# Performance work log

Hardware: AMD Instinct MI355X
Metric: run time of the kernel (lower is better)

The kernel has to match this reference:

```python
import jax, jax.numpy as jnp
import numpy as np

NUM_HEADS = 16

def rotate_half(x):
    h = x.shape[-1] // 2
    return jnp.concatenate([-x[..., h:], x[..., :h]], axis=-1)

def setup_inputs() -> dict:
    key = jax.random.key(0)
    k1, k2, k3 = jax.random.split(key, 3)
    B, S, H = 2, 2048, 1024
    x = jax.random.normal(k1, (B, S, H), dtype=jnp.float32)
    W_qkv = jax.random.normal(k2, (3 * H, H), dtype=jnp.float32) * (1.0 / np.sqrt(H))
    W_proj = jax.random.normal(k3, (H, H), dtype=jnp.float32) * (1.0 / np.sqrt(H))
    return {"x": x, "W_qkv": W_qkv, "W_proj": W_proj}

def reference(x, W_qkv, W_proj):
    B, S, H = x.shape
    nH = NUM_HEADS
    hd = H // nH
    # QKV projection (bias=False): y = x @ W.T
    qkv = jnp.einsum('bsh,oh->bso', x, W_qkv)  # [B,S,3H]
    q, k, v = jnp.split(qkv, 3, axis=-1)
    def to_heads(t):
        return t.reshape(B, S, nH, hd).transpose(0, 2, 1, 3)  # [B,nH,S,hd]
    q, k, v = to_heads(q), to_heads(k), to_heads(v)
    # RoPE on first half of head_dim; freqs dim = hd//2
    half = hd // 2
    inv_freq = 1.0 / (10000.0 ** (jnp.arange(0, hd, 2, dtype=jnp.float32) / hd))  # [hd//2]
    t = jnp.arange(S, dtype=jnp.float32)
    freqs = t[:, None] * inv_freq[None, :]  # [S, hd//2]
    cos = jnp.cos(freqs)[None, None]  # [1,1,S,hd//2]
    sin = jnp.sin(freqs)[None, None]
    q_half, q_rest = q[..., :half], q[..., half:]
    k_half, k_rest = k[..., :half], k[..., half:]
    q_rot = q_half * cos + rotate_half(q_half) * sin
    k_rot = k_half * cos + rotate_half(k_half) * sin
    q = jnp.concatenate([q_rot, q_rest], axis=-1)
    k = jnp.concatenate([k_rot, k_rest], axis=-1)
    # scaled dot-product attention (no mask, dropout=0 / eval)
    scale = 1.0 / np.sqrt(hd)
    att = jnp.einsum('bhqd,bhkd->bhqk', q, k) * scale  # [B,nH,S,S]
    att = jax.nn.softmax(att, axis=-1)
    out = jnp.einsum('bhqk,bhkd->bhqd', att, v)  # [B,nH,S,hd]
    out = out.transpose(0, 2, 1, 3).reshape(B, S, H)
    return jnp.einsum('bsh,oh->bso', out, W_proj)
```

## Files before the change

kernel.cpp:

```cpp
#include <hip/hip_runtime.h>
#include <math.h>

#define SEQ  2048
#define NHD  16
#define HD   64
#define HDIM 1024

typedef short s16x8 __attribute__((ext_vector_type(8)));
typedef short s16x4 __attribute__((ext_vector_type(4)));
typedef float f32x4 __attribute__((ext_vector_type(4)));

typedef const __attribute__((address_space(1))) unsigned int* gp_t;
typedef __attribute__((address_space(3))) unsigned int* lp_t;

__device__ __forceinline__ void async16(const short* g, short* l) {
    __builtin_amdgcn_global_load_lds((gp_t)g, (lp_t)l, 16, 0, 0);
}

__device__ __forceinline__ short f2bf(float f) {
    unsigned int u = __float_as_uint(f);
    u += 0x7fff + ((u >> 16) & 1);
    return (short)(u >> 16);
}
__device__ __forceinline__ float bf2f(short s) {
    return __uint_as_float(((unsigned int)(unsigned short)s) << 16);
}
__device__ __forceinline__ unsigned pkbf(float a, float b) {
    unsigned ua = __float_as_uint(a) + 0x8000u;
    unsigned ub = __float_as_uint(b) + 0x8000u;
    return __builtin_amdgcn_perm(ua, ub, 0x03020706u);
}

__global__ void detect_k(const unsigned short* __restrict__ x, int* __restrict__ flag) {
    int cnt = 0;
    #pragma unroll 4
    for (int j = 0; j < 32; ++j) {
        unsigned short h = x[threadIdx.x * 32 + j];
        int e = (h >> 7) & 0xFF;
        cnt += (e >= 100 && e <= 140) ? 1 : 0;
    }
    __shared__ int tot;
    if (threadIdx.x == 0) tot = 0;
    __syncthreads();
    atomicAdd(&tot, cnt);
    __syncthreads();
    if (threadIdx.x == 0) *flag = (tot > (8192 * 9) / 10) ? 1 : 0;
}

#define XG4  (4096 * 1024 / 4)
#define WQG4 (3072 * 1024 / 4)
#define WPG4 (1024 * 1024 / 4)
__global__ void cvt_all_k(const void* __restrict__ xr, const void* __restrict__ wqr,
                          const void* __restrict__ wpr, short* __restrict__ xo,
                          short* __restrict__ wqo, short* __restrict__ wpo,
                          const int* __restrict__ flag) {
    int i = blockIdx.x * 256 + threadIdx.x;
    const void* in; short* out; int j;
    if (i < XG4)             { in = xr;  out = xo;  j = i; }
    else if (i < XG4 + WQG4) { in = wqr; out = wqo; j = i - XG4; }
    else                     { in = wpr; out = wpo; j = i - XG4 - WQG4; }
    if (*flag) {
        ((s16x4*)out)[j] = ((const s16x4*)in)[j];
    } else {
        f32x4 v = ((const f32x4*)in)[j];
        union { unsigned u[2]; s16x4 v; } r;
        r.u[0] = pkbf(v[0], v[1]);
        r.u[1] = pkbf(v[2], v[3]);
        ((s16x4*)out)[j] = r.v;
    }
}

__global__ void rope_tab_k(float2* __restrict__ tab) {
    int i = blockIdx.x * 256 + threadIdx.x;
    if (i >= SEQ * 32) return;
    int s = i >> 5, d = i & 31;
    float invf = (float)pow(10000.0, -(double)d / 32.0);
    float af = (float)s * invf;
    double a = (double)af;
    tab[i] = make_float2((float)cos(a), (float)sin(a));
}

template<int MODE>
__global__ __launch_bounds__(256, 2)
void gemm_bt(const short* __restrict__ A, const short* __restrict__ B,
             short* __restrict__ q, short* __restrict__ kbuf, short* __restrict__ vt,
             float* __restrict__ C, const float2* __restrict__ tab,
             int K, int N) {
    __shared__ __align__(16) short As[2][128 * 32];
    __shared__ __align__(16) short Bs[2][128 * 32];
    const int tid  = threadIdx.x;
    const int w    = tid >> 6, lane = tid & 63;
    const int quad = lane >> 4, l16 = lane & 15;
    const int wm = (w >> 1) * 64, wn = (w & 1) * 64;
    const int rowA0 = blockIdx.y * 128;
    const int colB0 = blockIdx.x * 128;

    auto stage = [&](int buf, int kb) {
        #pragma unroll
        for (int i = 0; i < 2; ++i) {
            int cidx = i * 256 + w * 64 + lane;
            int row = cidx >> 2, sc = cidx & 3;
            int c = sc ^ (row & 3);
            async16(&A[(long)(rowA0 + row) * K + kb + c * 8],
                    &As[buf][(i * 256 + w * 64) * 8]);
            async16(&B[(long)(colB0 + row) * K + kb + c * 8],
                    &Bs[buf][(i * 256 + w * 64) * 8]);
        }
    };

    f32x4 acc[4][4] = {};
    stage(0, 0);

    for (int kb = 0, it = 0; kb < K; kb += 32, ++it) {
        const int cur = it & 1;
        __syncthreads();
        if (kb + 32 < K) stage(cur ^ 1, kb + 32);

        s16x8 af[4], bfr[4];
        const int slot = quad ^ (l16 & 3);
        #pragma unroll
        for (int mi = 0; mi < 4; ++mi)
            af[mi] = *(const s16x8*)&As[cur][(wm + mi * 16 + l16) * 32 + slot * 8];
        #pragma unroll
        for (int ni = 0; ni < 4; ++ni)
            bfr[ni] = *(const s16x8*)&Bs[cur][(wn + ni * 16 + l16) * 32 + slot * 8];
        #pragma unroll
        for (int mi = 0; mi < 4; ++mi)
            #pragma unroll
            for (int ni = 0; ni < 4; ++ni)
                acc[mi][ni] = __builtin_amdgcn_mfma_f32_16x16x32_bf16(
                    af[mi], bfr[ni], acc[mi][ni], 0, 0, 0);
    }

    const int cb = colB0 + wn;
    if (MODE == 1) {
        #pragma unroll
        for (int mi = 0; mi < 4; ++mi) {
            #pragma unroll
            for (int r = 0; r < 4; ++r) {
                int gm = rowA0 + wm + mi * 16 + quad * 4 + r;
                float* cp = C + (long)gm * N + cb + l16;
                #pragma unroll
                for (int ni = 0; ni < 4; ++ni)
                    cp[ni * 16] = acc[mi][ni][r];
            }
        }
        return;
    }
    const int sector = cb >> 10;
    const int head   = (cb & 1023) >> 6;
    const int gmb = rowA0 + wm;
    const int b = gmb >> 11, s0 = gmb & 2047;
    __syncthreads();
    short* arena = (w < 2) ? (&As[0][0] + w * 4096) : (&Bs[0][0] + (w - 2) * 4096);
    auto aw = [&](int row, int col, short val) {
        arena[row * 64 + (((col >> 3) ^ (row & 7)) << 3) + (col & 7)] = val;
    };
    if (sector < 2) {
        const float sc = (sector == 0) ? 0.18033688f : 1.0f;
        #pragma unroll
        for (int mi = 0; mi < 4; ++mi) {
            #pragma unroll
            for (int r = 0; r < 4; ++r) {
                int lrow = mi * 16 + quad * 4 + r;
                int s = s0 + lrow;
                float v0 = acc[mi][0][r], v1 = acc[mi][1][r];
                float v2 = acc[mi][2][r], v3 = acc[mi][3][r];
                float2 cs0 = tab[s * 32 + l16];
                float2 cs1 = tab[s * 32 + 16 + l16];
                float n0 = v0 * cs0.x - v1 * cs0.y;
                float n1 = v1 * cs1.x + v0 * cs1.y;
                aw(lrow, l16,      f2bf(n0 * sc));
                aw(lrow, l16 + 16, f2bf(n1 * sc));
                aw(lrow, l16 + 32, f2bf(v2 * sc));
                aw(lrow, l16 + 48, f2bf(v3 * sc));
            }
        }
        short* dst0 = (sector == 0 ? q : kbuf)
                    + ((long)((b * NHD + head) * SEQ + s0)) * HD;
        #pragma unroll
        for (int it = 0; it < 8; ++it) {
            int row = it * 8 + (lane >> 3), cc = lane & 7;
            s16x8 vv = *(const s16x8*)&arena[row * 64 + ((cc ^ (row & 7)) << 3)];
            *(s16x8*)&dst0[row * HD + cc * 8] = vv;
        }
    } else {
        #pragma unroll
        for (int mi = 0; mi < 4; ++mi) {
            #pragma unroll
            for (int r = 0; r < 4; ++r) {
                int scol = mi * 16 + quad * 4 + r;
                aw(l16,      scol, f2bf(acc[mi][0][r]));
                aw(l16 + 16, scol, f2bf(acc[mi][1][r]));
                aw(l16 + 32, scol, f2bf(acc[mi][2][r]));
                aw(l16 + 48, scol, f2bf(acc[mi][3][r]));
            }
        }
        short* dstv = vt + ((long)((b * NHD + head) * HD)) * SEQ + s0;
        #pragma unroll
        for (int it = 0; it < 8; ++it) {
            int dd = it * 8 + (lane >> 3), so8 = lane & 7;
            s16x8 vv = *(const s16x8*)&arena[dd * 64 + ((so8 ^ (dd & 7)) << 3)];
            *(s16x8*)&dstv[(long)dd * SEQ + so8 * 8] = vv;
        }
    }
}

__global__ __launch_bounds__(256, 4)
void flash_attn(const short* __restrict__ Q, const short* __restrict__ K,
                const short* __restrict__ Vt, short* __restrict__ opart,
                float* __restrict__ lpart, int nt) {
    __shared__ __align__(16) short Ks[2][64 * 64];
    __shared__ __align__(16) short Vs[2][64 * 64];
    const int tid  = threadIdx.x;
    const int w    = tid >> 6, lane = tid & 63;
    const int quad = lane >> 4, l16 = lane & 15;
    const int bh = blockIdx.x >> 1;
    const int z  = blockIdx.x & 1;
    const int qb = blockIdx.y * 128;
    const short* Qp = Q  + (long)bh * SEQ * HD + (long)qb * HD;
    const short* Kp = K  + (long)bh * SEQ * HD;
    const short* Vp = Vt + (long)bh * HD * SEQ;
    const int kt0 = z * nt;

    auto stage = [&](int buf, int kt) {
        #pragma unroll
        for (int i = 0; i < 2; ++i) {
            int cidx = i * 256 + w * 64 + lane;
            int row = cidx >> 3, sc = cidx & 7;
            int c = sc ^ (row & 7);
            async16(&Kp[(kt * 64 + row) * HD + c * 8],
                    &Ks[buf][(i * 256 + w * 64) * 8]);
            async16(&Vp[(long)row * SEQ + kt * 64 + c * 8],
                    &Vs[buf][(i * 256 + w * 64) * 8]);
        }
    };

    s16x8 aq[2][2];
    #pragma unroll
    for (int mi = 0; mi < 2; ++mi)
        #pragma unroll
        for (int ks = 0; ks < 2; ++ks)
            aq[mi][ks] = *(const s16x8*)&Qp[(w * 32 + mi * 16 + l16) * HD
                                            + ks * 32 + quad * 8];

    s16x8 ones8;
    #pragma unroll
    for (int j = 0; j < 8; ++j) ones8[j] = (short)0x3F80;

    f32x4 oacc[2][4] = {};
    f32x4 lacc[2] = {};

    stage(0, kt0);
    for (int it = 0; it < nt; ++it) {
        const int cur = it & 1;
        __syncthreads();
        if (it + 1 < nt) stage(cur ^ 1, kt0 + it + 1);

        f32x4 st[2][4] = {};
        #pragma unroll
        for (int ki = 0; ki < 4; ++ki) {
            s16x8 ak0 = *(const s16x8*)&Ks[cur][(ki * 16 + l16) * 64 + (quad ^ (l16 & 7)) * 8];
            s16x8 ak1 = *(const s16x8*)&Ks[cur][(ki * 16 + l16) * 64 + ((4 + quad) ^ (l16 & 7)) * 8];
            #pragma unroll
            for (int mi = 0; mi < 2; ++mi) {
                st[mi][ki] = __builtin_amdgcn_mfma_f32_16x16x32_bf16(
                    ak0, aq[mi][0], st[mi][ki], 0, 0, 0);
                st[mi][ki] = __builtin_amdgcn_mfma_f32_16x16x32_bf16(
                    ak1, aq[mi][1], st[mi][ki], 0, 0, 0);
            }
        }

        s16x8 bp[2][2];
        #pragma unroll
        for (int mi = 0; mi < 2; ++mi)
            #pragma unroll
            for (int t = 0; t < 2; ++t) {
                union { unsigned u[4]; s16x8 v; } pk;
                pk.u[0] = pkbf(exp2f(st[mi][2 * t][0]),     exp2f(st[mi][2 * t][1]));
                pk.u[1] = pkbf(exp2f(st[mi][2 * t][2]),     exp2f(st[mi][2 * t][3]));
                pk.u[2] = pkbf(exp2f(st[mi][2 * t + 1][0]), exp2f(st[mi][2 * t + 1][1]));
                pk.u[3] = pkbf(exp2f(st[mi][2 * t + 1][2]), exp2f(st[mi][2 * t + 1][3]));
                bp[mi][t] = pk.v;
            }

        #pragma unroll
        for (int t = 0; t < 2; ++t) {
            #pragma unroll
            for (int nd = 0; nd < 4; ++nd) {
                int d = nd * 16 + l16;
                s16x4 va = *(const s16x4*)&Vs[cur][d * 64
                             + ((4 * t + (quad >> 1)) ^ (l16 & 7)) * 8
                             + (quad & 1) * 4];
                s16x4 vb = *(const s16x4*)&Vs[cur][d * 64
                             + ((4 * t + 2 + (quad >> 1)) ^ (l16 & 7)) * 8
                             + (quad & 1) * 4];
                s16x8 av = {va[0], va[1], va[2], va[3],
                            vb[0], vb[1], vb[2], vb[3]};
                #pragma unroll
                for (int mi = 0; mi < 2; ++mi)
                    oacc[mi][nd] = __builtin_amdgcn_mfma_f32_16x16x32_bf16(
                        av, bp[mi][t], oacc[mi][nd], 0, 0, 0);
            }
            #pragma unroll
            for (int mi = 0; mi < 2; ++mi)
                lacc[mi] = __builtin_amdgcn_mfma_f32_16x16x32_bf16(
                    ones8, bp[mi][t], lacc[mi], 0, 0, 0);
        }
    }

    #pragma unroll
    for (int mi = 0; mi < 2; ++mi) {
        int srow = qb + w * 32 + mi * 16 + l16;
        long prow = (long)(z * 2 * NHD + bh) * SEQ + srow;
        if (quad == 0) lpart[prow] = lacc[mi][0];
        short* op = opart + prow * 64 + quad * 4;
        #pragma unroll
        for (int nd = 0; nd < 4; ++nd) {
            union { unsigned u[2]; s16x4 v; } pk;
            pk.u[0] = pkbf(oacc[mi][nd][0], oacc[mi][nd][1]);
            pk.u[1] = pkbf(oacc[mi][nd][2], oacc[mi][nd][3]);
            *(s16x4*)&op[nd * 16] = pk.v;
        }
    }
}

__global__ __launch_bounds__(256)
void merge_k(const short* __restrict__ opart, const float* __restrict__ lpart,
             short* __restrict__ att) {
    int idx = blockIdx.x * 256 + threadIdx.x;
    int t16 = idx & 15, rowg = idx >> 4;
    int bh = rowg >> 11, srow = rowg & 2047;
    float inv = 1.0f / (lpart[rowg] + lpart[65536 + rowg]);
    s16x4 o1 = *(const s16x4*)&opart[(long)rowg * 64 + t16 * 4];
    s16x4 o2 = *(const s16x4*)&opart[(long)(65536 + rowg) * 64 + t16 * 4];
    int b = bh >> 4, h = bh & 15;
    short* dst = att + ((long)(b * SEQ + srow)) * HDIM + h * HD + t16 * 4;
    union { unsigned u[2]; s16x4 v; } r;
    r.u[0] = pkbf((bf2f(o1[0]) + bf2f(o2[0])) * inv,
                  (bf2f(o1[1]) + bf2f(o2[1])) * inv);
    r.u[1] = pkbf((bf2f(o1[2]) + bf2f(o2[2])) * inv,
                  (bf2f(o1[3]) + bf2f(o2[3])) * inv);
    *(s16x4*)dst = r.v;
}

extern "C" void kernel_launch(void* const* d_in, const int* in_sizes, int n_in,
                              void* d_out, int out_size, void* d_ws, size_t ws_size,
                              hipStream_t stream) {
    const void* x_raw  = d_in[0];
    const void* Wq_raw = d_in[1];
    const void* Wp_raw = d_in[2];
    for (int i = 0; i < n_in; ++i) {
        if      (in_sizes[i] == 4096 * 1024) x_raw  = d_in[i];
        else if (in_sizes[i] == 3072 * 1024) Wq_raw = d_in[i];
        else if (in_sizes[i] == 1024 * 1024) Wp_raw = d_in[i];
    }
    float* out = (float*)d_out;

    const size_t MB = 1u << 20;
    char* ws = (char*)d_ws;
    short*  q     = (short*)(ws);
    short*  k     = (short*)(ws +  8 * MB);
    short*  vt    = (short*)(ws + 16 * MB);
    short*  xbf   = (short*)(ws + 24 * MB);
    short*  att   = xbf;
    short*  wqkv  = (short*)(ws + 32 * MB);
    short*  wprj  = (short*)(ws + 38 * MB);
    float2* tab   = (float2*)(ws + 40 * MB);
    int*    flag  = (int*)(ws + 40 * MB + 512 * 1024);
    short*  opart = (short*)(ws + 41 * MB);
    float*  lprt  = (float*)(ws + 57 * MB);

    detect_k<<<dim3(1), dim3(256), 0, stream>>>((const unsigned short*)x_raw, flag);

    cvt_all_k<<<dim3((XG4 + WQG4 + WPG4) / 256), dim3(256), 0, stream>>>(
        x_raw, Wq_raw, Wp_raw, xbf, wqkv, wprj, flag);

    rope_tab_k<<<dim3(SEQ * 32 / 256), dim3(256), 0, stream>>>(tab);

    gemm_bt<0><<<dim3(3072 / 128, 4096 / 128), dim3(256), 0, stream>>>(
        xbf, wqkv, q, k, vt, (float*)nullptr, tab, 1024, 3072);

    flash_attn<<<dim3(2 * NHD * 2, SEQ / 128), dim3(256), 0, stream>>>(
        q, k, vt, opart, lprt, 16);

    merge_k<<<dim3(65536 * 16 / 256), dim3(256), 0, stream>>>(opart, lprt, att);

    gemm_bt<1><<<dim3(1024 / 128, 4096 / 128), dim3(256), 0, stream>>>(
        att, wprj, (short*)nullptr, (short*)nullptr, (short*)nullptr, out, tab, 1024, 1024);
}
```

Before: 205.3 us.

## Fuse dtype detection, conversion and RoPE table into one kernel; trim attention inner loop

Merges the separate detect, convert and RoPE-table kernels into a single launch, with each conversion block deciding bf16-vs-fp32 input from a ballot over its own data instead of a global flag. This removes two kernel launches and their serialization. In flash attention the first MFMA of each score tile now takes a zero accumulator instead of a zero-initialised array, and exp2f is replaced by the raw hardware exp2 builtin. The per-block detection heuristic could classify blocks inconsistently, and the hardware exp2 may differ slightly in precision and denormal handling.

```diff
diff --git a/kernel.cpp b/kernel.cpp
--- a/kernel.cpp
+++ b/kernel.cpp
@@ -31,35 +31,38 @@
     return __builtin_amdgcn_perm(ua, ub, 0x03020706u);
 }
 
-__global__ void detect_k(const unsigned short* __restrict__ x, int* __restrict__ flag) {
-    int cnt = 0;
-    #pragma unroll 4
-    for (int j = 0; j < 32; ++j) {
-        unsigned short h = x[threadIdx.x * 32 + j];
-        int e = (h >> 7) & 0xFF;
-        cnt += (e >= 100 && e <= 140) ? 1 : 0;
-    }
-    __shared__ int tot;
-    if (threadIdx.x == 0) tot = 0;
-    __syncthreads();
-    atomicAdd(&tot, cnt);
-    __syncthreads();
-    if (threadIdx.x == 0) *flag = (tot > (8192 * 9) / 10) ? 1 : 0;
-}
-
 #define XG4  (4096 * 1024 / 4)
 #define WQG4 (3072 * 1024 / 4)
 #define WPG4 (1024 * 1024 / 4)
-__global__ void cvt_all_k(const void* __restrict__ xr, const void* __restrict__ wqr,
-                          const void* __restrict__ wpr, short* __restrict__ xo,
-                          short* __restrict__ wqo, short* __restrict__ wpo,
-                          const int* __restrict__ flag) {
-    int i = blockIdx.x * 256 + threadIdx.x;
+#define NCVT ((XG4 + WQG4 + WPG4) / 256)
+__global__ void cvt_rope_k(const void* __restrict__ xr, const void* __restrict__ wqr,
+                           const void* __restrict__ wpr, short* __restrict__ xo,
+                           short* __restrict__ wqo, short* __restrict__ wpo,
+                           float2* __restrict__ tab) {
+    const int tid = threadIdx.x;
+    if (blockIdx.x >= NCVT) {
+        int i = (blockIdx.x - NCVT) * 256 + tid;
+        int s = i >> 5, d = i & 31;
+        float invf = (float)pow(10000.0, -(double)d / 32.0);
+        float af = (float)s * invf;
+        tab[i] = make_float2((float)cos((double)af), (float)sin((double)af));
+        return;
+    }
+    int i = blockIdx.x * 256 + tid;
     const void* in; short* out; int j;
     if (i < XG4)             { in = xr;  out = xo;  j = i; }
     else if (i < XG4 + WQG4) { in = wqr; out = wqo; j = i - XG4; }
     else                     { in = wpr; out = wpo; j = i - XG4 - WQG4; }
-    if (*flag) {
+    const int jbase = j - tid;
+    unsigned short h = ((const unsigned short*)in)[(size_t)jbase * 4 + tid];
+    int e = (h >> 7) & 0xFF;
+    unsigned long long b = __ballot(e >= 100 && e <= 140);
+    __shared__ int tot;
+    if (tid == 0) tot = 0;
+    __syncthreads();
+    if ((tid & 63) == 0) atomicAdd(&tot, __popcll(b));
+    __syncthreads();
+    if (tot > 230) {
         ((s16x4*)out)[j] = ((const s16x4*)in)[j];
     } else {
         f32x4 v = ((const f32x4*)in)[j];
@@ -68,16 +71,6 @@
         r.u[1] = pkbf(v[2], v[3]);
         ((s16x4*)out)[j] = r.v;
     }
-}
-
-__global__ void rope_tab_k(float2* __restrict__ tab) {
-    int i = blockIdx.x * 256 + threadIdx.x;
-    if (i >= SEQ * 32) return;
-    int s = i >> 5, d = i & 31;
-    float invf = (float)pow(10000.0, -(double)d / 32.0);
-    float af = (float)s * invf;
-    double a = (double)af;
-    tab[i] = make_float2((float)cos(a), (float)sin(a));
 }
 
 template<int MODE>
@@ -248,6 +241,7 @@
     #pragma unroll
     for (int j = 0; j < 8; ++j) ones8[j] = (short)0x3F80;
 
+    const f32x4 z4 = {};
     f32x4 oacc[2][4] = {};
     f32x4 lacc[2] = {};
 
@@ -256,16 +250,18 @@
         const int cur = it & 1;
         __syncthreads();
         if (it + 1 < nt) stage(cur ^ 1, kt0 + it + 1);
-
-        f32x4 st[2][4] = {};
+        const short* kcur = Ks[cur];
+        const short* vcur = Vs[cur];
+
+        f32x4 st[2][4];
         #pragma unroll
         for (int ki = 0; ki < 4; ++ki) {
-            s16x8 ak0 = *(const s16x8*)&Ks[cur][(ki * 16 + l16) * 64 + (quad ^ (l16 & 7)) * 8];
-            s16x8 ak1 = *(const s16x8*)&Ks[cur][(ki * 16 + l16) * 64 + ((4 + quad) ^ (l16 & 7)) * 8];
+            s16x8 ak0 = *(const s16x8*)&kcur[(ki * 16 + l16) * 64 + (quad ^ (l16 & 7)) * 8];
+            s16x8 ak1 = *(const s16x8*)&kcur[(ki * 16 + l16) * 64 + ((4 + quad) ^ (l16 & 7)) * 8];
             #pragma unroll
             for (int mi = 0; mi < 2; ++mi) {
                 st[mi][ki] = __builtin_amdgcn_mfma_f32_16x16x32_bf16(
-                    ak0, aq[mi][0], st[mi][ki], 0, 0, 0);
+                    ak0, aq[mi][0], z4, 0, 0, 0);
                 st[mi][ki] = __builtin_amdgcn_mfma_f32_16x16x32_bf16(
                     ak1, aq[mi][1], st[mi][ki], 0, 0, 0);
             }
@@ -277,10 +273,14 @@
             #pragma unroll
             for (int t = 0; t < 2; ++t) {
                 union { unsigned u[4]; s16x8 v; } pk;
-                pk.u[0] = pkbf(exp2f(st[mi][2 * t][0]),     exp2f(st[mi][2 * t][1]));
-                pk.u[1] = pkbf(exp2f(st[mi][2 * t][2]),     exp2f(st[mi][2 * t][3]));
-                pk.u[2] = pkbf(exp2f(st[mi][2 * t + 1][0]), exp2f(st[mi][2 * t + 1][1]));
-                pk.u[3] = pkbf(exp2f(st[mi][2 * t + 1][2]), exp2f(st[mi][2 * t + 1][3]));
+                pk.u[0] = pkbf(__builtin_amdgcn_exp2f(st[mi][2 * t][0]),
+                               __builtin_amdgcn_exp2f(st[mi][2 * t][1]));
+                pk.u[1] = pkbf(__builtin_amdgcn_exp2f(st[mi][2 * t][2]),
+                               __builtin_amdgcn_exp2f(st[mi][2 * t][3]));
+                pk.u[2] = pkbf(__builtin_amdgcn_exp2f(st[mi][2 * t + 1][0]),
+                               __builtin_amdgcn_exp2f(st[mi][2 * t + 1][1]));
+                pk.u[3] = pkbf(__builtin_amdgcn_exp2f(st[mi][2 * t + 1][2]),
+                               __builtin_amdgcn_exp2f(st[mi][2 * t + 1][3]));
                 bp[mi][t] = pk.v;
             }
 
@@ -289,10 +289,10 @@
             #pragma unroll
             for (int nd = 0; nd < 4; ++nd) {
                 int d = nd * 16 + l16;
-                s16x4 va = *(const s16x4*)&Vs[cur][d * 64
+                s16x4 va = *(const s16x4*)&vcur[d * 64
                              + ((4 * t + (quad >> 1)) ^ (l16 & 7)) * 8
                              + (quad & 1) * 4];
-                s16x4 vb = *(const s16x4*)&Vs[cur][d * 64
+                s16x4 vb = *(const s16x4*)&vcur[d * 64
                              + ((4 * t + 2 + (quad >> 1)) ^ (l16 & 7)) * 8
                              + (quad & 1) * 4];
                 s16x8 av = {va[0], va[1], va[2], va[3],
@@ -367,16 +367,11 @@
     short*  wqkv  = (short*)(ws + 32 * MB);
     short*  wprj  = (short*)(ws + 38 * MB);
     float2* tab   = (float2*)(ws + 40 * MB);
-    int*    flag  = (int*)(ws + 40 * MB + 512 * 1024);
     short*  opart = (short*)(ws + 41 * MB);
     float*  lprt  = (float*)(ws + 57 * MB);
 
-    detect_k<<<dim3(1), dim3(256), 0, stream>>>((const unsigned short*)x_raw, flag);
-
-    cvt_all_k<<<dim3((XG4 + WQG4 + WPG4) / 256), dim3(256), 0, stream>>>(
-        x_raw, Wq_raw, Wp_raw, xbf, wqkv, wprj, flag);
-
-    rope_tab_k<<<dim3(SEQ * 32 / 256), dim3(256), 0, stream>>>(tab);
+    cvt_rope_k<<<dim3(NCVT + SEQ * 32 / 256), dim3(256), 0, stream>>>(
+        x_raw, Wq_raw, Wp_raw, xbf, wqkv, wprj, tab);
 
     gemm_bt<0><<<dim3(3072 / 128, 4096 / 128), dim3(256), 0, stream>>>(
         xbf, wqkv, q, k, vt, (float*)nullptr, tab, 1024, 3072);
```

Measured after the change: 191.3 us. 6.8% less time.
